# Performance work log

Measured on AMD Instinct MI355X. Metric: run time of the kernel, lower is better.

## Reference

```python
import jax, jax.numpy as jnp
import numpy as np

N_NODES = 50000
N_EDGES = 1000000
IN_DIM = 64
HID_DIM = 64
OUT_DIM = 8
N_GRAPHS = 64


def _glorot(key, shape):
    fan_in, fan_out = shape[0], shape[1]
    lim = float(np.sqrt(6.0 / (fan_in + fan_out)))
    return jax.random.uniform(key, shape, jnp.float32, -lim, lim)


def setup_inputs() -> dict:
    key = jax.random.key(0)
    ks = jax.random.split(key, 10)
    x = jax.random.normal(ks[0], (N_NODES, IN_DIM), jnp.float32)
    edge_index = jax.random.randint(ks[1], (2, N_EDGES), 0, N_NODES, jnp.int64)
    batch = jnp.sort(jax.random.randint(ks[2], (N_NODES,), 0, N_GRAPHS, jnp.int64))
    return {
        "x": x,
        "edge_index": edge_index,
        "batch": batch,
        # SAGEConv1: lin_l (applied to aggregated neighbors, has bias), lin_r (root)
        "W1_l": _glorot(ks[3], (IN_DIM, HID_DIM)),
        "b1": jnp.zeros((HID_DIM,), jnp.float32),
        "W1_r": _glorot(ks[4], (IN_DIM, HID_DIM)),
        # SAGEConv2
        "W2_l": _glorot(ks[5], (HID_DIM, HID_DIM)),
        "b2": jnp.zeros((HID_DIM,), jnp.float32),
        "W2_r": _glorot(ks[6], (HID_DIM, HID_DIM)),
        # final Linear
        "W_fc": _glorot(ks[7], (HID_DIM, OUT_DIM)),
        "b_fc": jnp.zeros((OUT_DIM,), jnp.float32),
    }


def _sage_conv(x, src, dst, W_l, b, W_r):
    # PyG SAGEConv (mean aggr): out = lin_l(mean_{j in N(i)} x_j) + lin_r(x_i)
    msg_sum = jax.ops.segment_sum(x[src], dst, num_segments=N_NODES)  # [N, d]
    deg = jax.ops.segment_sum(jnp.ones((src.shape[0],), x.dtype), dst,
                              num_segments=N_NODES)
    mean = msg_sum / jnp.maximum(deg, 1.0)[:, None]
    return mean @ W_l + b + x @ W_r


def reference(x, edge_index, batch, W1_l, b1, W1_r, W2_l, b2, W2_r, W_fc, b_fc):
    src, dst = edge_index[0], edge_index[1]
    h = jax.nn.relu(_sage_conv(x, src, dst, W1_l, b1, W1_r))
    h = jax.nn.relu(_sage_conv(h, src, dst, W2_l, b2, W2_r))
    # global_mean_pool over graph ids
    pooled_sum = jax.ops.segment_sum(h, batch, num_segments=N_GRAPHS)  # [G, d]
    counts = jax.ops.segment_sum(jnp.ones((N_NODES,), h.dtype), batch,
                                 num_segments=N_GRAPHS)
    pooled = pooled_sum / jnp.maximum(counts, 1.0)[:, None]
    return pooled @ W_fc + b_fc
```

## Files before the change

kernel.cpp:

```cpp
#include <hip/hip_runtime.h>
#include <hip/hip_bf16.h>

#define N_NODES 50000
#define N_EDGES 1000000
#define DIM 64
#define N_GRAPHS 64
#define OUT_DIM 8
#define NBLK_SCAN 196
#define NPART 8
#define SUBBLK 16
#define NODES_PER_PART (N_NODES / NPART)
#define NB_RP 512
#define CHUNK_E4 489
#define B_STRIDE 8192
#define POOL_NPW 64

typedef __attribute__((ext_vector_type(8))) short short8;
typedef __attribute__((ext_vector_type(4))) float f32x4;
typedef __attribute__((ext_vector_type(4))) int v4i;

__device__ __forceinline__ unsigned short f2b(float f) {
    __hip_bfloat16 h = __float2bfloat16(f);
    return *reinterpret_cast<unsigned short*>(&h);
}
__device__ __forceinline__ float b2f(unsigned short u) {
    __hip_bfloat16 h = *reinterpret_cast<__hip_bfloat16*>(&u);
    return __bfloat162float(h);
}

__global__ void histB_kernel(const int* __restrict__ dst, int* __restrict__ blockcnt) {
    __shared__ int sc[NPART];
    if (threadIdx.x < NPART) sc[threadIdx.x] = 0;
    __syncthreads();

    int e4lo = blockIdx.x * CHUNK_E4;
    int e4hi = e4lo + CHUNK_E4; if (e4hi > N_EDGES / 4) e4hi = N_EDGES / 4;

    int c0 = 0, c1 = 0, c2 = 0, c3 = 0, c4 = 0, c5 = 0, c6 = 0, c7 = 0;
    for (int e4 = e4lo + threadIdx.x; e4 < e4hi; e4 += 256) {
        v4i d = ((const v4i*)dst)[e4];
#define CNT1(DD)                                                              \
        {                                                                     \
            unsigned p = (unsigned)(DD) / NODES_PER_PART;                     \
            c0 += (p == 0); c1 += (p == 1); c2 += (p == 2); c3 += (p == 3);   \
            c4 += (p == 4); c5 += (p == 5); c6 += (p == 6); c7 += (p == 7);   \
        }
        CNT1(d.x) CNT1(d.y) CNT1(d.z) CNT1(d.w)
#undef CNT1
    }
    #pragma unroll
    for (int off = 32; off > 0; off >>= 1) {
        c0 += __shfl_xor(c0, off); c1 += __shfl_xor(c1, off);
        c2 += __shfl_xor(c2, off); c3 += __shfl_xor(c3, off);
        c4 += __shfl_xor(c4, off); c5 += __shfl_xor(c5, off);
        c6 += __shfl_xor(c6, off); c7 += __shfl_xor(c7, off);
    }
    if ((threadIdx.x & 63) == 0) {
        atomicAdd(&sc[0], c0); atomicAdd(&sc[1], c1);
        atomicAdd(&sc[2], c2); atomicAdd(&sc[3], c3);
        atomicAdd(&sc[4], c4); atomicAdd(&sc[5], c5);
        atomicAdd(&sc[6], c6); atomicAdd(&sc[7], c7);
    }
    __syncthreads();
    if (threadIdx.x < NPART) blockcnt[blockIdx.x * NPART + threadIdx.x] = sc[threadIdx.x];
}

__global__ void scan8_kernel(const int* __restrict__ blockcnt,
                             int* __restrict__ abs_off, int* __restrict__ bucket_base) {
    __shared__ int part[1024];
    int t = threadIdx.x;
    int v[4], s = 0;
    #pragma unroll
    for (int i = 0; i < 4; ++i) {
        int e = 4 * t + i;
        int p = e >> 9, b = e & (NB_RP - 1);
        v[i] = blockcnt[b * NPART + p];
        s += v[i];
    }
    part[t] = s;
    __syncthreads();
    for (int off = 1; off < 1024; off <<= 1) {
        int u = (t >= off) ? part[t - off] : 0;
        __syncthreads();
        part[t] += u;
        __syncthreads();
    }
    int base = (t == 0) ? 0 : part[t - 1];
    #pragma unroll
    for (int i = 0; i < 4; ++i) {
        int e = 4 * t + i;
        abs_off[e] = base;
        if (i == 0 && (t & 127) == 0) bucket_base[t >> 7] = base;
        base += v[i];
    }
    if (t == 1023) bucket_base[NPART] = N_EDGES;
}

__global__ void scatterP_kernel(const int* __restrict__ src, const int* __restrict__ dst,
                                const int* __restrict__ abs_off,
                                int* __restrict__ db, int* __restrict__ sb) {
    __shared__ int lcur[NPART];
    if (threadIdx.x < NPART)
        lcur[threadIdx.x] = abs_off[threadIdx.x * NB_RP + blockIdx.x];
    __syncthreads();

    int e4lo = blockIdx.x * CHUNK_E4;
    int e4hi = e4lo + CHUNK_E4; if (e4hi > N_EDGES / 4) e4hi = N_EDGES / 4;

    for (int e4 = e4lo + threadIdx.x; e4 < e4hi; e4 += 256) {
        v4i d = ((const v4i*)dst)[e4];
        v4i s = ((const v4i*)src)[e4];
#define PUT1(DD, SS)                                                          \
        {                                                                     \
            unsigned p = (unsigned)(DD) / NODES_PER_PART;                     \
            int pos = atomicAdd(&lcur[p], 1);                                 \
            db[pos] = (DD); sb[pos] = (SS);                                   \
        }
        PUT1(d.x, s.x) PUT1(d.y, s.y) PUT1(d.z, s.z) PUT1(d.w, s.w)
#undef PUT1
    }
}

__global__ void count_priv_kernel(const int* __restrict__ db,
                                  const int* __restrict__ bucket_base,
                                  int* __restrict__ privhist) {
    __shared__ int lh[NODES_PER_PART];
    int p = blockIdx.x & (NPART - 1);
    int sub = blockIdx.x >> 3;
    for (int i = threadIdx.x; i < NODES_PER_PART; i += 256) lh[i] = 0;
    __syncthreads();

    int lo = bucket_base[p], hi = bucket_base[p + 1];
    int len = hi - lo;
    int chunk = (len + SUBBLK - 1) / SUBBLK;
    int clo = lo + sub * chunk;
    int chi = clo + chunk; if (chi > hi) chi = hi;
    int nbase = p * NODES_PER_PART;

    for (int i = clo + threadIdx.x; i < chi; i += 256)
        atomicAdd(&lh[db[i] - nbase], 1);
    __syncthreads();

    int* o = privhist + (size_t)blockIdx.x * NODES_PER_PART;
    for (int i = threadIdx.x; i < NODES_PER_PART; i += 256) o[i] = lh[i];
}

__global__ void merge_hist_kernel(int* __restrict__ privhist, int* __restrict__ cnt,
                                  int* __restrict__ bsum) {
    __shared__ int sd[256];
    int t = threadIdx.x;
    int n = blockIdx.x * 256 + t;
    int run = 0;
    if (n < N_NODES) {
        int p = n / NODES_PER_PART;
        int nl = n - p * NODES_PER_PART;
        #pragma unroll
        for (int b = 0; b < SUBBLK; ++b) {
            size_t idx = (size_t)(b * NPART + p) * NODES_PER_PART + nl;
            int v = privhist[idx];
            privhist[idx] = run;
            run += v;
        }
        cnt[n] = run;
    }
    sd[t] = (n < N_NODES) ? run : 0;
    __syncthreads();
    for (int off = 128; off > 0; off >>= 1) {
        if (t < off) sd[t] += sd[t + off];
        __syncthreads();
    }
    if (t == 0) bsum[blockIdx.x] = sd[0];
}

__global__ void scan_bsum_kernel(const int* __restrict__ bsum, int* __restrict__ boff,
                                 int* __restrict__ row_start) {
    __shared__ int sd[256];
    int t = threadIdx.x;
    int v = (t < NBLK_SCAN) ? bsum[t] : 0;
    sd[t] = v;
    __syncthreads();
    for (int off = 1; off < 256; off <<= 1) {
        int u = (t >= off) ? sd[t - off] : 0;
        __syncthreads();
        sd[t] += u;
        __syncthreads();
    }
    if (t < NBLK_SCAN) boff[t] = sd[t] - v;
    if (t == 0) row_start[N_NODES] = N_EDGES;
}

__global__ void scan_write_kernel(const int* __restrict__ cnt, const int* __restrict__ boff,
                                  int* __restrict__ row_start) {
    __shared__ int sd[256];
    int t = threadIdx.x;
    int idx = blockIdx.x * 256 + t;
    int v = (idx < N_NODES) ? cnt[idx] : 0;
    sd[t] = v;
    __syncthreads();
    for (int off = 1; off < 256; off <<= 1) {
        int u = (t >= off) ? sd[t - off] : 0;
        __syncthreads();
        sd[t] += u;
        __syncthreads();
    }
    if (idx < N_NODES) row_start[idx] = sd[t] - v + boff[blockIdx.x];
}

__global__ void fill_det_kernel(const int* __restrict__ db, const int* __restrict__ sb,
                                const int* __restrict__ bucket_base,
                                const int* __restrict__ row_start,
                                const int* __restrict__ privhist,
                                int* __restrict__ csr) {
    __shared__ int cur[NODES_PER_PART];
    int p = blockIdx.x & (NPART - 1);
    int sub = blockIdx.x >> 3;
    int nbase = p * NODES_PER_PART;
    const int* ph = privhist + (size_t)blockIdx.x * NODES_PER_PART;
    for (int i = threadIdx.x; i < NODES_PER_PART; i += 256)
        cur[i] = row_start[nbase + i] + ph[i];
    __syncthreads();

    int lo = bucket_base[p], hi = bucket_base[p + 1];
    int len = hi - lo;
    int chunk = (len + SUBBLK - 1) / SUBBLK;
    int clo = lo + sub * chunk;
    int chi = clo + chunk; if (chi > hi) chi = hi;

    for (int i = clo + threadIdx.x; i < chi; i += 256) {
        int d = db[i];
        int s = sb[i];
        int pos = atomicAdd(&cur[d - nbase], 1);
        csr[pos] = s;
    }
}

__global__ void xcvt_kernel(const float* __restrict__ x, unsigned short* __restrict__ xb) {
    int i = blockIdx.x * 256 + threadIdx.x;
    if (i >= N_NODES * DIM / 4) return;
    float4 v = ((const float4*)x)[i];
    ushort4 u;
    u.x = f2b(v.x); u.y = f2b(v.y); u.z = f2b(v.z); u.w = f2b(v.w);
    ((ushort4*)xb)[i] = u;
}

__global__ void prep_b_kernel(const float* __restrict__ W1l, const float* __restrict__ W1r,
                              const float* __restrict__ W2l, const float* __restrict__ W2r,
                              unsigned short* __restrict__ Bf) {
    int t = blockIdx.x * 256 + threadIdx.x;
    if (t >= 2048) return;
    int layer = t >> 10;
    int rem = t & 1023;
    int ks = rem >> 8;
    int nt = (rem >> 6) & 3;
    int lane = rem & 63;
    int gq = lane >> 4;
    int col = nt * 16 + (lane & 15);
    const float* Wl = layer ? W2l : W1l;
    const float* Wr = layer ? W2r : W1r;
    unsigned short* o = Bf + (size_t)layer * B_STRIDE + ((ks * 4 + nt) * 64 + lane) * 8;
    #pragma unroll
    for (int i = 0; i < 8; ++i) {
        int k = ks * 32 + gq * 8 + i;
        float v = (k < DIM) ? Wl[k * DIM + col] : Wr[(k - DIM) * DIM + col];
        o[i] = f2b(v);
    }
}

__global__ __launch_bounds__(256) void mean_b_kernel(const unsigned short* __restrict__ feat,
                                                     const int* __restrict__ row_start,
                                                     const int* __restrict__ csr,
                                                     unsigned short* __restrict__ mean) {
    int wv = (blockIdx.x * blockDim.x + threadIdx.x) >> 6;
    if (wv >= N_NODES) return;
    int lane = threadIdx.x & 63;
    int grp = lane >> 4;
    int fi = lane & 15;
    int rs = row_start[wv], re = row_start[wv + 1];

    float4 a0 = make_float4(0.f, 0.f, 0.f, 0.f);
    float4 a1 = make_float4(0.f, 0.f, 0.f, 0.f);
    int i = rs;
    for (; i + 8 <= re; i += 8) {
        int s0 = csr[i + grp];
        int s1 = csr[i + 4 + grp];
        ushort4 u0 = ((const ushort4*)(feat + (size_t)s0 * DIM))[fi];
        ushort4 u1 = ((const ushort4*)(feat + (size_t)s1 * DIM))[fi];
        a0.x += b2f(u0.x); a0.y += b2f(u0.y); a0.z += b2f(u0.z); a0.w += b2f(u0.w);
        a1.x += b2f(u1.x); a1.y += b2f(u1.y); a1.z += b2f(u1.z); a1.w += b2f(u1.w);
    }
    if (i + 4 <= re) {
        int s = csr[i + grp];
        ushort4 u = ((const ushort4*)(feat + (size_t)s * DIM))[fi];
        a0.x += b2f(u.x); a0.y += b2f(u.y); a0.z += b2f(u.z); a0.w += b2f(u.w);
        i += 4;
    }
    if (i + grp < re) {
        int s = csr[i + grp];
        ushort4 u = ((const ushort4*)(feat + (size_t)s * DIM))[fi];
        a1.x += b2f(u.x); a1.y += b2f(u.y); a1.z += b2f(u.z); a1.w += b2f(u.w);
    }
    float4 acc = make_float4(a0.x + a1.x, a0.y + a1.y, a0.z + a1.z, a0.w + a1.w);

    acc.x += __shfl_xor(acc.x, 16); acc.y += __shfl_xor(acc.y, 16);
    acc.z += __shfl_xor(acc.z, 16); acc.w += __shfl_xor(acc.w, 16);
    acc.x += __shfl_xor(acc.x, 32); acc.y += __shfl_xor(acc.y, 32);
    acc.z += __shfl_xor(acc.z, 32); acc.w += __shfl_xor(acc.w, 32);

    if (grp == 0) {
        float inv = 1.0f / fmaxf((float)(re - rs), 1.0f);
        ushort4 m;
        m.x = f2b(acc.x * inv); m.y = f2b(acc.y * inv);
        m.z = f2b(acc.z * inv); m.w = f2b(acc.w * inv);
        ((ushort4*)(mean + (size_t)wv * DIM))[fi] = m;
    }
}

__global__ __launch_bounds__(256, 2) void gemm_kernel(
        const unsigned short* __restrict__ Am,
        const unsigned short* __restrict__ Ax,
        const unsigned short* __restrict__ Bf,
        const float* __restrict__ bias,
        unsigned short* __restrict__ outb) {
    int wv = (blockIdx.x * blockDim.x + threadIdx.x) >> 6;
    int n0 = wv * 16;
    if (n0 >= N_NODES) return;
    int lane = threadIdx.x & 63;
    int g = lane >> 4;
    int r = lane & 15;

    const short8* Bv = (const short8*)Bf;
    short8 b00 = Bv[ 0 * 64 + lane], b01 = Bv[ 1 * 64 + lane],
           b02 = Bv[ 2 * 64 + lane], b03 = Bv[ 3 * 64 + lane];
    short8 b10 = Bv[ 4 * 64 + lane], b11 = Bv[ 5 * 64 + lane],
           b12 = Bv[ 6 * 64 + lane], b13 = Bv[ 7 * 64 + lane];
    short8 b20 = Bv[ 8 * 64 + lane], b21 = Bv[ 9 * 64 + lane],
           b22 = Bv[10 * 64 + lane], b23 = Bv[11 * 64 + lane];
    short8 b30 = Bv[12 * 64 + lane], b31 = Bv[13 * 64 + lane],
           b32 = Bv[14 * 64 + lane], b33 = Bv[15 * 64 + lane];

    f32x4 acc0 = {0.f, 0.f, 0.f, 0.f}, acc1 = {0.f, 0.f, 0.f, 0.f};
    f32x4 acc2 = {0.f, 0.f, 0.f, 0.f}, acc3 = {0.f, 0.f, 0.f, 0.f};

    const unsigned short* a1p = Am + (size_t)(n0 + r) * DIM + g * 8;
    const unsigned short* a2p = Ax + (size_t)(n0 + r) * DIM + g * 8;

    short8 a;
    a = *(const short8*)(a1p);
    acc0 = __builtin_amdgcn_mfma_f32_16x16x32_bf16(a, b00, acc0, 0, 0, 0);
    acc1 = __builtin_amdgcn_mfma_f32_16x16x32_bf16(a, b01, acc1, 0, 0, 0);
    acc2 = __builtin_amdgcn_mfma_f32_16x16x32_bf16(a, b02, acc2, 0, 0, 0);
    acc3 = __builtin_amdgcn_mfma_f32_16x16x32_bf16(a, b03, acc3, 0, 0, 0);
    a = *(const short8*)(a1p + 32);
    acc0 = __builtin_amdgcn_mfma_f32_16x16x32_bf16(a, b10, acc0, 0, 0, 0);
    acc1 = __builtin_amdgcn_mfma_f32_16x16x32_bf16(a, b11, acc1, 0, 0, 0);
    acc2 = __builtin_amdgcn_mfma_f32_16x16x32_bf16(a, b12, acc2, 0, 0, 0);
    acc3 = __builtin_amdgcn_mfma_f32_16x16x32_bf16(a, b13, acc3, 0, 0, 0);
    a = *(const short8*)(a2p);
    acc0 = __builtin_amdgcn_mfma_f32_16x16x32_bf16(a, b20, acc0, 0, 0, 0);
    acc1 = __builtin_amdgcn_mfma_f32_16x16x32_bf16(a, b21, acc1, 0, 0, 0);
    acc2 = __builtin_amdgcn_mfma_f32_16x16x32_bf16(a, b22, acc2, 0, 0, 0);
    acc3 = __builtin_amdgcn_mfma_f32_16x16x32_bf16(a, b23, acc3, 0, 0, 0);
    a = *(const short8*)(a2p + 32);
    acc0 = __builtin_amdgcn_mfma_f32_16x16x32_bf16(a, b30, acc0, 0, 0, 0);
    acc1 = __builtin_amdgcn_mfma_f32_16x16x32_bf16(a, b31, acc1, 0, 0, 0);
    acc2 = __builtin_amdgcn_mfma_f32_16x16x32_bf16(a, b32, acc2, 0, 0, 0);
    acc3 = __builtin_amdgcn_mfma_f32_16x16x32_bf16(a, b33, acc3, 0, 0, 0);

    int base_row = n0 + 4 * g;
#define EPI(NT, ACC)                                                          \
    {                                                                         \
        float bc = bias[(NT) * 16 + r];                                       \
        _Pragma("unroll")                                                     \
        for (int i = 0; i < 4; ++i) {                                         \
            float v = fmaxf(ACC[i] + bc, 0.0f);                               \
            outb[(size_t)(base_row + i) * DIM + (NT) * 16 + r] = f2b(v);      \
        }                                                                     \
    }
    EPI(0, acc0) EPI(1, acc1) EPI(2, acc2) EPI(3, acc3)
#undef EPI
}

__global__ void pool_b_kernel(const unsigned short* __restrict__ h,
                              const int* __restrict__ batch,
                              float* __restrict__ psum, float* __restrict__ pcnt) {
    int wv = (blockIdx.x * blockDim.x + threadIdx.x) >> 6;
    int start = wv * POOL_NPW;
    if (start >= N_NODES) return;
    int j = threadIdx.x & 63;
    int end = start + POOL_NPW;
    if (end > N_NODES) end = N_NODES;

    int g = batch[start];
    float acc = 0.0f, cnt = 0.0f;
    for (int n = start; n < end; ++n) {
        int gn = batch[n];
        if (gn != g) {
            atomicAdd(&psum[g * DIM + j], acc);
            if (j == 0) atomicAdd(&pcnt[g], cnt);
            g = gn; acc = 0.0f; cnt = 0.0f;
        }
        acc += b2f(h[(size_t)n * DIM + j]);
        cnt += 1.0f;
    }
    atomicAdd(&psum[g * DIM + j], acc);
    if (j == 0) atomicAdd(&pcnt[g], cnt);
}

__global__ void fc_kernel(const float* __restrict__ psum,
                          const float* __restrict__ pcnt,
                          const float* __restrict__ Wfc,
                          const float* __restrict__ bfc,
                          float* __restrict__ out) {
    int tid = threadIdx.x;
    if (tid >= N_GRAPHS * OUT_DIM) return;
    int g = tid >> 3;
    int o = tid & 7;
    float inv = 1.0f / fmaxf(pcnt[g], 1.0f);
    float s = bfc[o];
    #pragma unroll
    for (int k = 0; k < DIM; ++k) {
        s += psum[g * DIM + k] * inv * Wfc[k * OUT_DIM + o];
    }
    out[g * OUT_DIM + o] = s;
}

extern "C" void kernel_launch(void* const* d_in, const int* in_sizes, int n_in,
                              void* d_out, int out_size, void* d_ws, size_t ws_size,
                              hipStream_t stream) {
    const float* x   = (const float*)d_in[0];
    const int* ei    = (const int*)d_in[1];
    const int* batch = (const int*)d_in[2];
    const float* W1l = (const float*)d_in[3];
    const float* b1  = (const float*)d_in[4];
    const float* W1r = (const float*)d_in[5];
    const float* W2l = (const float*)d_in[6];
    const float* b2  = (const float*)d_in[7];
    const float* W2r = (const float*)d_in[8];
    const float* Wfc = (const float*)d_in[9];
    const float* bfc = (const float*)d_in[10];
    float* out = (float*)d_out;

    const int* src = ei;
    const int* dst = ei + N_EDGES;

    const size_t SZ_BF   = (size_t)N_NODES * DIM * 2;
    const size_t SZ_CSR  = (size_t)N_EDGES * sizeof(int);
    const size_t SZ_CNT  = ((size_t)(N_NODES + 1) * sizeof(int) + 255) & ~(size_t)255;
    char* ws = (char*)d_ws;
    int*   csr       = (int*)(ws);
    int*   cnt       = (int*)(ws + SZ_CSR);
    int*   row_start = (int*)(ws + SZ_CSR + SZ_CNT);
    char*  tail      = ws + SZ_CSR + 2 * SZ_CNT;
    int*   bsum      = (int*)(tail);
    int*   boff      = bsum + 256;
    int*   blockcnt  = boff + 256;
    int*   abs_off   = blockcnt + NB_RP * NPART;
    int*   bucket_base = abs_off + NB_RP * NPART;
    unsigned short* Bf = (unsigned short*)(bucket_base + 16);
    float* psum      = (float*)((char*)Bf + 2 * B_STRIDE * 2);
    float* pcnt      = psum + N_GRAPHS * DIM;
    char*  regionA   = (char*)(pcnt + N_GRAPHS) + 4096;
    regionA = (char*)(((size_t)regionA + 255) & ~(size_t)255);
    int*   db        = (int*)(regionA);
    int*   sb        = (int*)(regionA + SZ_CSR);
    int*   privhist  = (int*)(regionA + 2 * SZ_CSR);
    unsigned short* xb    = (unsigned short*)(regionA);
    unsigned short* meanb = (unsigned short*)(regionA + SZ_BF);
    unsigned short* h1b   = (unsigned short*)(regionA + 2 * SZ_BF);
    unsigned short* h2b   = (unsigned short*)(regionA + 3 * SZ_BF);

    const int meanBlocks  = (N_NODES + 3) / 4;
    const int tileWaves   = (N_NODES + 15) / 16;
    const int tileBlocks  = (tileWaves + 3) / 4;
    const int xcvtBlocks  = (N_NODES * DIM / 4 + 255) / 256;
    const int poolWaves   = (N_NODES + POOL_NPW - 1) / POOL_NPW;
    const int poolBlocks  = (poolWaves + 3) / 4;

    hipMemsetAsync(psum, 0, (size_t)(N_GRAPHS * DIM + N_GRAPHS) * sizeof(float), stream);

    histB_kernel<<<NB_RP, 256, 0, stream>>>(dst, blockcnt);
    scan8_kernel<<<1, 1024, 0, stream>>>(blockcnt, abs_off, bucket_base);
    scatterP_kernel<<<NB_RP, 256, 0, stream>>>(src, dst, abs_off, db, sb);
    count_priv_kernel<<<NPART * SUBBLK, 256, 0, stream>>>(db, bucket_base, privhist);
    merge_hist_kernel<<<NBLK_SCAN, 256, 0, stream>>>(privhist, cnt, bsum);
    scan_bsum_kernel<<<1, 256, 0, stream>>>(bsum, boff, row_start);
    scan_write_kernel<<<NBLK_SCAN, 256, 0, stream>>>(cnt, boff, row_start);
    fill_det_kernel<<<NPART * SUBBLK, 256, 0, stream>>>(db, sb, bucket_base, row_start,
                                                        privhist, csr);

    xcvt_kernel<<<xcvtBlocks, 256, 0, stream>>>(x, xb);
    prep_b_kernel<<<8, 256, 0, stream>>>(W1l, W1r, W2l, W2r, Bf);

    mean_b_kernel<<<meanBlocks, 256, 0, stream>>>(xb, row_start, csr, meanb);
    gemm_kernel<<<tileBlocks, 256, 0, stream>>>(meanb, xb, Bf, b1, h1b);
    mean_b_kernel<<<meanBlocks, 256, 0, stream>>>(h1b, row_start, csr, meanb);
    gemm_kernel<<<tileBlocks, 256, 0, stream>>>(meanb, h1b, Bf + B_STRIDE, b2, h2b);
    pool_b_kernel<<<poolBlocks, 256, 0, stream>>>(h2b, batch, psum, pcnt);
    fc_kernel<<<1, 512, 0, stream>>>(psum, pcnt, Wfc, bfc, out);
}
```

Before: 162.3 us.

## Fuse neighbor mean aggregation with SAGE MFMA GEMM via LDS tile

Merges the per-layer mean aggregation kernel and the MFMA GEMM kernel into one kernel. Each 256-thread block gathers means for 16 nodes into shared memory, then each wave computes one 16-column output tile with MFMA. This removes the global round-trip of the mean buffer and two kernel launches per forward pass. In exchange, each wave now processes 4 nodes serially, and the block barrier can leave waves idle when node degrees are uneven. The GEMM is also split across waves by output column, so every wave reloads the root-feature A rows.

```diff
diff --git a/kernel.cpp b/kernel.cpp
--- a/kernel.cpp
+++ b/kernel.cpp
@@ -14,6 +14,7 @@
 #define CHUNK_E4 489
 #define B_STRIDE 8192
 #define POOL_NPW 64
+#define LMPAD 80
 
 typedef __attribute__((ext_vector_type(8))) short short8;
 typedef __attribute__((ext_vector_type(4))) float f32x4;
@@ -266,118 +267,90 @@
     }
 }
 
-__global__ __launch_bounds__(256) void mean_b_kernel(const unsigned short* __restrict__ feat,
-                                                     const int* __restrict__ row_start,
-                                                     const int* __restrict__ csr,
-                                                     unsigned short* __restrict__ mean) {
-    int wv = (blockIdx.x * blockDim.x + threadIdx.x) >> 6;
-    if (wv >= N_NODES) return;
+__global__ __launch_bounds__(256) void sage_fused_kernel(
+        const unsigned short* __restrict__ feat,
+        const int* __restrict__ row_start,
+        const int* __restrict__ csr,
+        const unsigned short* __restrict__ Bf,
+        const float* __restrict__ bias,
+        unsigned short* __restrict__ outb) {
+    __shared__ unsigned short lmean[16][LMPAD];
+    int n0 = blockIdx.x * 16;
+    int wid = threadIdx.x >> 6;
     int lane = threadIdx.x & 63;
     int grp = lane >> 4;
     int fi = lane & 15;
-    int rs = row_start[wv], re = row_start[wv + 1];
-
-    float4 a0 = make_float4(0.f, 0.f, 0.f, 0.f);
-    float4 a1 = make_float4(0.f, 0.f, 0.f, 0.f);
-    int i = rs;
-    for (; i + 8 <= re; i += 8) {
-        int s0 = csr[i + grp];
-        int s1 = csr[i + 4 + grp];
-        ushort4 u0 = ((const ushort4*)(feat + (size_t)s0 * DIM))[fi];
-        ushort4 u1 = ((const ushort4*)(feat + (size_t)s1 * DIM))[fi];
-        a0.x += b2f(u0.x); a0.y += b2f(u0.y); a0.z += b2f(u0.z); a0.w += b2f(u0.w);
-        a1.x += b2f(u1.x); a1.y += b2f(u1.y); a1.z += b2f(u1.z); a1.w += b2f(u1.w);
-    }
-    if (i + 4 <= re) {
-        int s = csr[i + grp];
-        ushort4 u = ((const ushort4*)(feat + (size_t)s * DIM))[fi];
-        a0.x += b2f(u.x); a0.y += b2f(u.y); a0.z += b2f(u.z); a0.w += b2f(u.w);
-        i += 4;
-    }
-    if (i + grp < re) {
-        int s = csr[i + grp];
-        ushort4 u = ((const ushort4*)(feat + (size_t)s * DIM))[fi];
-        a1.x += b2f(u.x); a1.y += b2f(u.y); a1.z += b2f(u.z); a1.w += b2f(u.w);
-    }
-    float4 acc = make_float4(a0.x + a1.x, a0.y + a1.y, a0.z + a1.z, a0.w + a1.w);
-
-    acc.x += __shfl_xor(acc.x, 16); acc.y += __shfl_xor(acc.y, 16);
-    acc.z += __shfl_xor(acc.z, 16); acc.w += __shfl_xor(acc.w, 16);
-    acc.x += __shfl_xor(acc.x, 32); acc.y += __shfl_xor(acc.y, 32);
-    acc.z += __shfl_xor(acc.z, 32); acc.w += __shfl_xor(acc.w, 32);
-
-    if (grp == 0) {
-        float inv = 1.0f / fmaxf((float)(re - rs), 1.0f);
-        ushort4 m;
-        m.x = f2b(acc.x * inv); m.y = f2b(acc.y * inv);
-        m.z = f2b(acc.z * inv); m.w = f2b(acc.w * inv);
-        ((ushort4*)(mean + (size_t)wv * DIM))[fi] = m;
-    }
-}
-
-__global__ __launch_bounds__(256, 2) void gemm_kernel(
-        const unsigned short* __restrict__ Am,
-        const unsigned short* __restrict__ Ax,
-        const unsigned short* __restrict__ Bf,
-        const float* __restrict__ bias,
-        unsigned short* __restrict__ outb) {
-    int wv = (blockIdx.x * blockDim.x + threadIdx.x) >> 6;
-    int n0 = wv * 16;
-    if (n0 >= N_NODES) return;
-    int lane = threadIdx.x & 63;
+
+    for (int rr = 0; rr < 4; ++rr) {
+        int n = n0 + 4 * wid + rr;
+        int rs = row_start[n], re = row_start[n + 1];
+
+        float4 a0 = make_float4(0.f, 0.f, 0.f, 0.f);
+        float4 a1 = make_float4(0.f, 0.f, 0.f, 0.f);
+        int i = rs;
+        for (; i + 8 <= re; i += 8) {
+            int s0 = csr[i + grp];
+            int s1 = csr[i + 4 + grp];
+            ushort4 u0 = ((const ushort4*)(feat + (size_t)s0 * DIM))[fi];
+            ushort4 u1 = ((const ushort4*)(feat + (size_t)s1 * DIM))[fi];
+            a0.x += b2f(u0.x); a0.y += b2f(u0.y); a0.z += b2f(u0.z); a0.w += b2f(u0.w);
+            a1.x += b2f(u1.x); a1.y += b2f(u1.y); a1.z += b2f(u1.z); a1.w += b2f(u1.w);
+        }
+        if (i + 4 <= re) {
+            int s = csr[i + grp];
+            ushort4 u = ((const ushort4*)(feat + (size_t)s * DIM))[fi];
+            a0.x += b2f(u.x); a0.y += b2f(u.y); a0.z += b2f(u.z); a0.w += b2f(u.w);
+            i += 4;
+        }
+        if (i + grp < re) {
+            int s = csr[i + grp];
+            ushort4 u = ((const ushort4*)(feat + (size_t)s * DIM))[fi];
+            a1.x += b2f(u.x); a1.y += b2f(u.y); a1.z += b2f(u.z); a1.w += b2f(u.w);
+        }
+        float4 acc = make_float4(a0.x + a1.x, a0.y + a1.y, a0.z + a1.z, a0.w + a1.w);
+
+        acc.x += __shfl_xor(acc.x, 16); acc.y += __shfl_xor(acc.y, 16);
+        acc.z += __shfl_xor(acc.z, 16); acc.w += __shfl_xor(acc.w, 16);
+        acc.x += __shfl_xor(acc.x, 32); acc.y += __shfl_xor(acc.y, 32);
+        acc.z += __shfl_xor(acc.z, 32); acc.w += __shfl_xor(acc.w, 32);
+
+        if (grp == 0) {
+            float inv = 1.0f / fmaxf((float)(re - rs), 1.0f);
+            ushort4 m;
+            m.x = f2b(acc.x * inv); m.y = f2b(acc.y * inv);
+            m.z = f2b(acc.z * inv); m.w = f2b(acc.w * inv);
+            ((ushort4*)&lmean[4 * wid + rr][0])[fi] = m;
+        }
+    }
+    __syncthreads();
+
+    const short8* Bv = (const short8*)Bf;
+    short8 bk0 = Bv[(0 * 4 + wid) * 64 + lane];
+    short8 bk1 = Bv[(1 * 4 + wid) * 64 + lane];
+    short8 bk2 = Bv[(2 * 4 + wid) * 64 + lane];
+    short8 bk3 = Bv[(3 * 4 + wid) * 64 + lane];
+
     int g = lane >> 4;
     int r = lane & 15;
-
-    const short8* Bv = (const short8*)Bf;
-    short8 b00 = Bv[ 0 * 64 + lane], b01 = Bv[ 1 * 64 + lane],
-           b02 = Bv[ 2 * 64 + lane], b03 = Bv[ 3 * 64 + lane];
-    short8 b10 = Bv[ 4 * 64 + lane], b11 = Bv[ 5 * 64 + lane],
-           b12 = Bv[ 6 * 64 + lane], b13 = Bv[ 7 * 64 + lane];
-    short8 b20 = Bv[ 8 * 64 + lane], b21 = Bv[ 9 * 64 + lane],
-           b22 = Bv[10 * 64 + lane], b23 = Bv[11 * 64 + lane];
-    short8 b30 = Bv[12 * 64 + lane], b31 = Bv[13 * 64 + lane],
-           b32 = Bv[14 * 64 + lane], b33 = Bv[15 * 64 + lane];
-
-    f32x4 acc0 = {0.f, 0.f, 0.f, 0.f}, acc1 = {0.f, 0.f, 0.f, 0.f};
-    f32x4 acc2 = {0.f, 0.f, 0.f, 0.f}, acc3 = {0.f, 0.f, 0.f, 0.f};
-
-    const unsigned short* a1p = Am + (size_t)(n0 + r) * DIM + g * 8;
-    const unsigned short* a2p = Ax + (size_t)(n0 + r) * DIM + g * 8;
+    f32x4 acc = {0.f, 0.f, 0.f, 0.f};
 
     short8 a;
-    a = *(const short8*)(a1p);
-    acc0 = __builtin_amdgcn_mfma_f32_16x16x32_bf16(a, b00, acc0, 0, 0, 0);
-    acc1 = __builtin_amdgcn_mfma_f32_16x16x32_bf16(a, b01, acc1, 0, 0, 0);
-    acc2 = __builtin_amdgcn_mfma_f32_16x16x32_bf16(a, b02, acc2, 0, 0, 0);
-    acc3 = __builtin_amdgcn_mfma_f32_16x16x32_bf16(a, b03, acc3, 0, 0, 0);
-    a = *(const short8*)(a1p + 32);
-    acc0 = __builtin_amdgcn_mfma_f32_16x16x32_bf16(a, b10, acc0, 0, 0, 0);
-    acc1 = __builtin_amdgcn_mfma_f32_16x16x32_bf16(a, b11, acc1, 0, 0, 0);
-    acc2 = __builtin_amdgcn_mfma_f32_16x16x32_bf16(a, b12, acc2, 0, 0, 0);
-    acc3 = __builtin_amdgcn_mfma_f32_16x16x32_bf16(a, b13, acc3, 0, 0, 0);
-    a = *(const short8*)(a2p);
-    acc0 = __builtin_amdgcn_mfma_f32_16x16x32_bf16(a, b20, acc0, 0, 0, 0);
-    acc1 = __builtin_amdgcn_mfma_f32_16x16x32_bf16(a, b21, acc1, 0, 0, 0);
-    acc2 = __builtin_amdgcn_mfma_f32_16x16x32_bf16(a, b22, acc2, 0, 0, 0);
-    acc3 = __builtin_amdgcn_mfma_f32_16x16x32_bf16(a, b23, acc3, 0, 0, 0);
-    a = *(const short8*)(a2p + 32);
-    acc0 = __builtin_amdgcn_mfma_f32_16x16x32_bf16(a, b30, acc0, 0, 0, 0);
-    acc1 = __builtin_amdgcn_mfma_f32_16x16x32_bf16(a, b31, acc1, 0, 0, 0);
-    acc2 = __builtin_amdgcn_mfma_f32_16x16x32_bf16(a, b32, acc2, 0, 0, 0);
-    acc3 = __builtin_amdgcn_mfma_f32_16x16x32_bf16(a, b33, acc3, 0, 0, 0);
-
-    int base_row = n0 + 4 * g;
-#define EPI(NT, ACC)                                                          \
-    {                                                                         \
-        float bc = bias[(NT) * 16 + r];                                       \
-        _Pragma("unroll")                                                     \
-        for (int i = 0; i < 4; ++i) {                                         \
-            float v = fmaxf(ACC[i] + bc, 0.0f);                               \
-            outb[(size_t)(base_row + i) * DIM + (NT) * 16 + r] = f2b(v);      \
-        }                                                                     \
-    }
-    EPI(0, acc0) EPI(1, acc1) EPI(2, acc2) EPI(3, acc3)
-#undef EPI
+    a = *(const short8*)&lmean[r][g * 8];
+    acc = __builtin_amdgcn_mfma_f32_16x16x32_bf16(a, bk0, acc, 0, 0, 0);
+    a = *(const short8*)&lmean[r][32 + g * 8];
+    acc = __builtin_amdgcn_mfma_f32_16x16x32_bf16(a, bk1, acc, 0, 0, 0);
+    const unsigned short* axp = feat + (size_t)(n0 + r) * DIM + g * 8;
+    a = *(const short8*)(axp);
+    acc = __builtin_amdgcn_mfma_f32_16x16x32_bf16(a, bk2, acc, 0, 0, 0);
+    a = *(const short8*)(axp + 32);
+    acc = __builtin_amdgcn_mfma_f32_16x16x32_bf16(a, bk3, acc, 0, 0, 0);
+
+    float bc = bias[wid * 16 + r];
+    #pragma unroll
+    for (int i = 0; i < 4; ++i) {
+        float v = fmaxf(acc[i] + bc, 0.0f);
+        outb[(size_t)(n0 + 4 * g + i) * DIM + wid * 16 + r] = f2b(v);
+    }
 }
 
 __global__ void pool_b_kernel(const unsigned short* __restrict__ h,
@@ -465,13 +438,10 @@
     int*   sb        = (int*)(regionA + SZ_CSR);
     int*   privhist  = (int*)(regionA + 2 * SZ_CSR);
     unsigned short* xb    = (unsigned short*)(regionA);
-    unsigned short* meanb = (unsigned short*)(regionA + SZ_BF);
-    unsigned short* h1b   = (unsigned short*)(regionA + 2 * SZ_BF);
-    unsigned short* h2b   = (unsigned short*)(regionA + 3 * SZ_BF);
-
-    const int meanBlocks  = (N_NODES + 3) / 4;
-    const int tileWaves   = (N_NODES + 15) / 16;
-    const int tileBlocks  = (tileWaves + 3) / 4;
+    unsigned short* h1b   = (unsigned short*)(regionA + SZ_BF);
+    unsigned short* h2b   = (unsigned short*)(regionA + 2 * SZ_BF);
+
+    const int fusedBlocks = N_NODES / 16;
     const int xcvtBlocks  = (N_NODES * DIM / 4 + 255) / 256;
     const int poolWaves   = (N_NODES + POOL_NPW - 1) / POOL_NPW;
     const int poolBlocks  = (poolWaves + 3) / 4;
@@ -491,10 +461,9 @@
     xcvt_kernel<<<xcvtBlocks, 256, 0, stream>>>(x, xb);
     prep_b_kernel<<<8, 256, 0, stream>>>(W1l, W1r, W2l, W2r, Bf);
 
-    mean_b_kernel<<<meanBlocks, 256, 0, stream>>>(xb, row_start, csr, meanb);
-    gemm_kernel<<<tileBlocks, 256, 0, stream>>>(meanb, xb, Bf, b1, h1b);
-    mean_b_kernel<<<meanBlocks, 256, 0, stream>>>(h1b, row_start, csr, meanb);
-    gemm_kernel<<<tileBlocks, 256, 0, stream>>>(meanb, h1b, Bf + B_STRIDE, b2, h2b);
+    sage_fused_kernel<<<fusedBlocks, 256, 0, stream>>>(xb, row_start, csr, Bf, b1, h1b);
+    sage_fused_kernel<<<fusedBlocks, 256, 0, stream>>>(h1b, row_start, csr,
+                                                       Bf + B_STRIDE, b2, h2b);
     pool_b_kernel<<<poolBlocks, 256, 0, stream>>>(h2b, batch, psum, pcnt);
     fc_kernel<<<1, 512, 0, stream>>>(psum, pcnt, Wfc, bfc, out);
 }
```

Result: no change. 160.7 us (-1.0%).
